# Optimization experiments

Hardware: AMD Instinct MI355X
Metric: run time of the kernel (lower is better)

Reference implementation:

```python
import jax, jax.numpy as jnp
import numpy as np

T, C, H, W, D = 100, 2, 128, 128, 8192


def setup_inputs() -> dict:
    key = jax.random.key(0)
    k1, k2, k3, k4 = jax.random.split(key, 4)
    # event histogram: nonnegative intensities per (time, polarity, y, x)
    hist = jax.random.uniform(k1, (T, C, H, W), dtype=jnp.float32)
    # torchhd Random(vsa='MAP') tables are random bipolar {-1,+1} vectors
    time_w = jnp.sign(jax.random.normal(k2, (T, D), dtype=jnp.float32))
    pol_w = jnp.sign(jax.random.normal(k3, (C, D), dtype=jnp.float32))
    pos_w = jnp.sign(jax.random.normal(k4, (H * W, D), dtype=jnp.float32))
    return {"hist": hist, "time_w": time_w, "pol_w": pol_w, "pos_w": pos_w}


def reference(hist, time_w, pol_w, pos_w):
    # Original: for every nonzero pixel, bind (elementwise mul in MAP)
    # pos_hv * pol_hv * time_hv, scale by intensity, accumulate, then sign.
    # Equivalent fused form:
    #   out_d = sign( sum_{t,p,n} hist[t,p,n] * pos_w[n,d] * pol_w[p,d] * time_w[t,d] )
    t, c, h, w = hist.shape
    flat = hist.reshape(t, c, h * w)                      # [T, 2, H*W]
    # intensity-weighted sum of position HVs per (t, p): one GEMM over H*W
    acc = jnp.einsum('tpn,nd->tpd', flat, pos_w)          # [T, 2, D]
    # bind with polarity and time HVs, reduce over t and p
    gesture = jnp.einsum('tpd,pd,td->d', acc, pol_w, time_w)  # [D]
    return jnp.sign(gesture)
```

## Files before the change

### kernel.cpp

```cpp
#include <hip/hip_runtime.h>
#include <cstdint>
#include <cstddef>

#define TT    100
#define MROWS 200
#define KDIM  16384
#define DDIM  8192
#define KSL   16
#define KPER  (KDIM / KSL)

typedef __bf16 bf16x8 __attribute__((ext_vector_type(8)));
typedef float  f32x4  __attribute__((ext_vector_type(4)));

static __device__ __forceinline__ unsigned short f2bf_rne(float f) {
    unsigned int u = __float_as_uint(f);
    unsigned int r = (u + 0x7FFFu + ((u >> 16) & 1u)) >> 16;
    return (unsigned short)r;
}
static __device__ __forceinline__ float bf2f(unsigned short s) {
    return __uint_as_float(((unsigned int)s) << 16);
}

__global__ __launch_bounds__(256) void zero_kernel(float* __restrict__ out) {
    out[blockIdx.x * 256 + threadIdx.x] = 0.f;
}

__global__ __launch_bounds__(256) void gemm_kernel(const float* __restrict__ hist,
                                                   const float* __restrict__ pos,
                                                   const float* __restrict__ time_w,
                                                   const float* __restrict__ pol_w,
                                                   float* __restrict__ out) {
    __shared__ alignas(16) unsigned short As[2][128][32];
    __shared__ alignas(16) unsigned short Bs[128][40];
    __shared__ float sPart[128];

    const int t     = threadIdx.x;
    const int n0    = blockIdx.x * 128;
    const int m0    = blockIdx.y * 128;
    const int kbase = blockIdx.z * KPER;

    const int lane = t & 63;
    const int wv   = t >> 6;
    const int wm   = (wv & 1) * 64;
    const int wn   = (wv >> 1) * 64;
    const int l15  = lane & 15;
    const int q8   = (lane >> 4) * 8;

    if (t < 128) sPart[t] = 0.f;

    const int ar  = t >> 2;
    const int akb = (t & 3) * 8;
    const int rowA0 = m0 + ar;
    const int rowA1 = m0 + ar + 64;
    const bool v0 = rowA0 < MROWS;
    const bool v1 = rowA1 < MROWS;
    const float* gA0 = hist + (size_t)rowA0 * KDIM + akb;
    const float* gA1 = hist + (size_t)rowA1 * KDIM + akb;

    const int bk2 = (t & 15) * 2;
    const int bnb = (t >> 4) * 8;
    const float* gB0 = pos + ((size_t)kbase + bk2) * DDIM + n0 + bnb;
    const float* gB1 = gB0 + DDIM;

    f32x4 acc[4][4];
#pragma unroll
    for (int s = 0; s < 4; ++s)
#pragma unroll
        for (int j = 0; j < 4; ++j) acc[s][j] = (f32x4){0.f, 0.f, 0.f, 0.f};

    for (int kk = 0; kk < KPER; kk += 32) {
        float4 a00 = {0,0,0,0}, a01 = {0,0,0,0};
        float4 a10 = {0,0,0,0}, a11 = {0,0,0,0};
        if (v0) { a00 = *(const float4*)(gA0 + kbase + kk);
                  a01 = *(const float4*)(gA0 + kbase + kk + 4); }
        if (v1) { a10 = *(const float4*)(gA1 + kbase + kk);
                  a11 = *(const float4*)(gA1 + kbase + kk + 4); }
        const float* b0 = gB0 + (size_t)kk * DDIM;
        const float* b1 = gB1 + (size_t)kk * DDIM;
        float4 x0 = *(const float4*)(b0);
        float4 x1 = *(const float4*)(b0 + 4);
        float4 y0 = *(const float4*)(b1);
        float4 y1 = *(const float4*)(b1 + 4);

        __syncthreads();

        {
            float va[8] = {a00.x, a00.y, a00.z, a00.w, a01.x, a01.y, a01.z, a01.w};
            float vb[8] = {a10.x, a10.y, a10.z, a10.w, a11.x, a11.y, a11.z, a11.w};
            alignas(16) unsigned short h0[8], l0[8], h1[8], l1[8];
#pragma unroll
            for (int i = 0; i < 8; ++i) {
                unsigned short h = f2bf_rne(va[i]);
                h0[i] = h; l0[i] = f2bf_rne(va[i] - bf2f(h));
                unsigned short g = f2bf_rne(vb[i]);
                h1[i] = g; l1[i] = f2bf_rne(vb[i] - bf2f(g));
            }
            *(uint4*)&As[0][ar][akb]      = *(const uint4*)h0;
            *(uint4*)&As[1][ar][akb]      = *(const uint4*)l0;
            *(uint4*)&As[0][ar + 64][akb] = *(const uint4*)h1;
            *(uint4*)&As[1][ar + 64][akb] = *(const uint4*)l1;
        }
        {
            const float xv[8] = {x0.x, x0.y, x0.z, x0.w, x1.x, x1.y, x1.z, x1.w};
            const float yv[8] = {y0.x, y0.y, y0.z, y0.w, y1.x, y1.y, y1.z, y1.w};
#pragma unroll
            for (int j = 0; j < 8; ++j) {
                unsigned int w = (__float_as_uint(xv[j]) >> 16) |
                                 (__float_as_uint(yv[j]) & 0xFFFF0000u);
                *(unsigned int*)&Bs[bnb + j][bk2] = w;
            }
        }

        __syncthreads();

        uint4 fa0[4], fa1[4], fb[4];
#pragma unroll
        for (int s = 0; s < 4; ++s) {
            fa0[s] = *(const uint4*)&As[0][wm + s * 16 + l15][q8];
            fa1[s] = *(const uint4*)&As[1][wm + s * 16 + l15][q8];
        }
#pragma unroll
        for (int j = 0; j < 4; ++j)
            fb[j] = *(const uint4*)&Bs[wn + j * 16 + l15][q8];

#pragma unroll
        for (int s = 0; s < 4; ++s)
#pragma unroll
            for (int j = 0; j < 4; ++j) {
                acc[s][j] = __builtin_amdgcn_mfma_f32_16x16x32_bf16(
                    __builtin_bit_cast(bf16x8, fa0[s]),
                    __builtin_bit_cast(bf16x8, fb[j]), acc[s][j], 0, 0, 0);
                acc[s][j] = __builtin_amdgcn_mfma_f32_16x16x32_bf16(
                    __builtin_bit_cast(bf16x8, fa1[s]),
                    __builtin_bit_cast(bf16x8, fb[j]), acc[s][j], 0, 0, 0);
            }
    }

    const int qrow = (lane >> 4) * 4;
#pragma unroll
    for (int j = 0; j < 4; ++j) {
        const int col = wn + j * 16 + l15;
        const int d   = n0 + col;
        const float p0 = pol_w[d];
        const float p1 = pol_w[DDIM + d];
        float part = 0.f;
#pragma unroll
        for (int s = 0; s < 4; ++s)
#pragma unroll
            for (int r = 0; r < 4; ++r) {
                const int m = m0 + wm + s * 16 + qrow + r;
                if (m < MROWS) {
                    const int tt_ = m >> 1;
                    const float w = time_w[(size_t)tt_ * DDIM + d] *
                                    ((m & 1) ? p1 : p0);
                    part += w * acc[s][j][r];
                }
            }
        atomicAdd(&sPart[col], part);
    }
    __syncthreads();
    if (t < 128) atomicAdd(out + n0 + t, sPart[t]);
}

__global__ __launch_bounds__(256) void sign_kernel(float* __restrict__ out) {
    int d = blockIdx.x * 256 + threadIdx.x;
    float s = out[d];
    out[d] = (s > 0.f) ? 1.f : ((s < 0.f) ? -1.f : 0.f);
}

extern "C" void kernel_launch(void* const* d_in, const int* in_sizes, int n_in,
                              void* d_out, int out_size, void* d_ws, size_t ws_size,
                              hipStream_t stream) {
    const float* hist   = (const float*)d_in[0];
    const float* time_w = (const float*)d_in[1];
    const float* pol_w  = (const float*)d_in[2];
    const float* pos_w  = (const float*)d_in[3];
    float* out = (float*)d_out;
    (void)d_ws; (void)ws_size;

    zero_kernel<<<DDIM / 256, 256, 0, stream>>>(out);
    gemm_kernel<<<dim3(DDIM / 128, 2, KSL), 256, 0, stream>>>(hist, pos_w, time_w, pol_w, out);
    sign_kernel<<<DDIM / 256, 256, 0, stream>>>(out);
}
```

Baseline: 767.7 us.

## Precompute bf16 hi/lo split of hist and cover all M rows per block

A new prep kernel converts hist once into swizzled bf16 hi/lo planes padded to 224 rows in workspace. The GEMM then tiles all rows in a single block (M=224), so pos_w is streamed once instead of twice, and the A tiles are loaded directly into LDS with global_load_lds, using an XOR swizzle to avoid bank conflicts. The grid is reordered so k-slices vary fastest. The cost is an extra kernel launch plus a workspace round trip, and a larger accumulator (7x4 tiles) that raises register pressure.

```diff
diff --git a/kernel.cpp b/kernel.cpp
--- a/kernel.cpp
+++ b/kernel.cpp
@@ -2,12 +2,13 @@
 #include <cstdint>
 #include <cstddef>
 
-#define TT    100
 #define MROWS 200
+#define PM    224
 #define KDIM  16384
 #define DDIM  8192
 #define KSL   16
 #define KPER  (KDIM / KSL)
+#define BK    32
 
 typedef __bf16 bf16x8 __attribute__((ext_vector_type(8)));
 typedef float  f32x4  __attribute__((ext_vector_type(4)));
@@ -21,60 +22,96 @@
     return __uint_as_float(((unsigned int)s) << 16);
 }
 
+static __device__ __forceinline__ void gld_lds16(const unsigned short* g,
+                                                 unsigned short* l) {
+    __builtin_amdgcn_global_load_lds(
+        (const __attribute__((address_space(1))) unsigned int*)g,
+        (__attribute__((address_space(3))) unsigned int*)l, 16, 0, 0);
+}
+
 __global__ __launch_bounds__(256) void zero_kernel(float* __restrict__ out) {
     out[blockIdx.x * 256 + threadIdx.x] = 0.f;
 }
 
-__global__ __launch_bounds__(256) void gemm_kernel(const float* __restrict__ hist,
-                                                   const float* __restrict__ pos,
-                                                   const float* __restrict__ time_w,
-                                                   const float* __restrict__ pol_w,
-                                                   float* __restrict__ out) {
-    __shared__ alignas(16) unsigned short As[2][128][32];
+__global__ __launch_bounds__(256) void prep_kernel(const float* __restrict__ hist,
+                                                   unsigned short* __restrict__ ahi,
+                                                   unsigned short* __restrict__ alo) {
+    const int g  = blockIdx.x * 256 + threadIdx.x;
+    const int m  = g >> 11;
+    const int gc = g & 2047;
+    const int f  = (m >> 1) & 3;
+    const int sgc = (gc & ~3) | ((gc & 3) ^ f);
+    alignas(16) unsigned short hi[8], lo[8];
+    if (m < MROWS) {
+        const float* src = hist + (size_t)m * KDIM + sgc * 8;
+        float4 a = *(const float4*)(src);
+        float4 b = *(const float4*)(src + 4);
+        const float v[8] = {a.x, a.y, a.z, a.w, b.x, b.y, b.z, b.w};
+#pragma unroll
+        for (int i = 0; i < 8; ++i) {
+            unsigned short h = f2bf_rne(v[i]);
+            hi[i] = h;
+            lo[i] = f2bf_rne(v[i] - bf2f(h));
+        }
+    } else {
+#pragma unroll
+        for (int i = 0; i < 8; ++i) { hi[i] = 0; lo[i] = 0; }
+    }
+    *(uint4*)(ahi + (size_t)g * 8) = *(const uint4*)hi;
+    *(uint4*)(alo + (size_t)g * 8) = *(const uint4*)lo;
+}
+
+__global__ __launch_bounds__(256, 2)
+void gemm_kernel(const unsigned short* __restrict__ ahi,
+                 const unsigned short* __restrict__ alo,
+                 const float* __restrict__ pos,
+                 const float* __restrict__ time_w,
+                 const float* __restrict__ pol_w,
+                 float* __restrict__ out) {
+    __shared__ alignas(16) unsigned short As0[PM * BK];
+    __shared__ alignas(16) unsigned short As1[PM * BK];
     __shared__ alignas(16) unsigned short Bs[128][40];
     __shared__ float sPart[128];
 
     const int t     = threadIdx.x;
-    const int n0    = blockIdx.x * 128;
-    const int m0    = blockIdx.y * 128;
-    const int kbase = blockIdx.z * KPER;
+    const int ks    = blockIdx.x;
+    const int n0    = blockIdx.y * 128;
+    const int kbase = ks * KPER;
 
     const int lane = t & 63;
     const int wv   = t >> 6;
-    const int wm   = (wv & 1) * 64;
+    const int wm   = (wv & 1) * 112;
     const int wn   = (wv >> 1) * 64;
     const int l15  = lane & 15;
     const int q8   = (lane >> 4) * 8;
+    const int qg   = (lane >> 4) ^ ((l15 >> 1) & 3);
 
     if (t < 128) sPart[t] = 0.f;
 
-    const int ar  = t >> 2;
-    const int akb = (t & 3) * 8;
-    const int rowA0 = m0 + ar;
-    const int rowA1 = m0 + ar + 64;
-    const bool v0 = rowA0 < MROWS;
-    const bool v1 = rowA1 < MROWS;
-    const float* gA0 = hist + (size_t)rowA0 * KDIM + akb;
-    const float* gA1 = hist + (size_t)rowA1 * KDIM + akb;
+    const int lr = lane >> 2, lg = lane & 3;
+    const unsigned short* gA[7];
+    unsigned short* lA[7];
+#pragma unroll
+    for (int i = 0; i < 7; ++i) {
+        const int cc = wv * 7 + i;
+        const int pl = (cc >= 14) ? 1 : 0;
+        const int ch = cc - pl * 14;
+        gA[i] = (pl ? alo : ahi) + (size_t)(ch * 16 + lr) * KDIM + kbase + lg * 8;
+        lA[i] = (pl ? As1 : As0) + ch * 512;
+    }
 
     const int bk2 = (t & 15) * 2;
     const int bnb = (t >> 4) * 8;
     const float* gB0 = pos + ((size_t)kbase + bk2) * DDIM + n0 + bnb;
     const float* gB1 = gB0 + DDIM;
 
-    f32x4 acc[4][4];
-#pragma unroll
-    for (int s = 0; s < 4; ++s)
+    f32x4 acc[7][4];
+#pragma unroll
+    for (int s = 0; s < 7; ++s)
 #pragma unroll
         for (int j = 0; j < 4; ++j) acc[s][j] = (f32x4){0.f, 0.f, 0.f, 0.f};
 
-    for (int kk = 0; kk < KPER; kk += 32) {
-        float4 a00 = {0,0,0,0}, a01 = {0,0,0,0};
-        float4 a10 = {0,0,0,0}, a11 = {0,0,0,0};
-        if (v0) { a00 = *(const float4*)(gA0 + kbase + kk);
-                  a01 = *(const float4*)(gA0 + kbase + kk + 4); }
-        if (v1) { a10 = *(const float4*)(gA1 + kbase + kk);
-                  a11 = *(const float4*)(gA1 + kbase + kk + 4); }
+    for (int kk = 0; kk < KPER; kk += BK) {
         const float* b0 = gB0 + (size_t)kk * DDIM;
         const float* b1 = gB1 + (size_t)kk * DDIM;
         float4 x0 = *(const float4*)(b0);
@@ -84,22 +121,9 @@
 
         __syncthreads();
 
-        {
-            float va[8] = {a00.x, a00.y, a00.z, a00.w, a01.x, a01.y, a01.z, a01.w};
-            float vb[8] = {a10.x, a10.y, a10.z, a10.w, a11.x, a11.y, a11.z, a11.w};
-            alignas(16) unsigned short h0[8], l0[8], h1[8], l1[8];
-#pragma unroll
-            for (int i = 0; i < 8; ++i) {
-                unsigned short h = f2bf_rne(va[i]);
-                h0[i] = h; l0[i] = f2bf_rne(va[i] - bf2f(h));
-                unsigned short g = f2bf_rne(vb[i]);
-                h1[i] = g; l1[i] = f2bf_rne(vb[i] - bf2f(g));
-            }
-            *(uint4*)&As[0][ar][akb]      = *(const uint4*)h0;
-            *(uint4*)&As[1][ar][akb]      = *(const uint4*)l0;
-            *(uint4*)&As[0][ar + 64][akb] = *(const uint4*)h1;
-            *(uint4*)&As[1][ar + 64][akb] = *(const uint4*)l1;
-        }
+#pragma unroll
+        for (int i = 0; i < 7; ++i) gld_lds16(gA[i] + kk, lA[i]);
+
         {
             const float xv[8] = {x0.x, x0.y, x0.z, x0.w, x1.x, x1.y, x1.z, x1.w};
             const float yv[8] = {y0.x, y0.y, y0.z, y0.w, y1.x, y1.y, y1.z, y1.w};
@@ -113,27 +137,26 @@
 
         __syncthreads();
 
-        uint4 fa0[4], fa1[4], fb[4];
-#pragma unroll
-        for (int s = 0; s < 4; ++s) {
-            fa0[s] = *(const uint4*)&As[0][wm + s * 16 + l15][q8];
-            fa1[s] = *(const uint4*)&As[1][wm + s * 16 + l15][q8];
-        }
+        uint4 fb[4];
 #pragma unroll
         for (int j = 0; j < 4; ++j)
             fb[j] = *(const uint4*)&Bs[wn + j * 16 + l15][q8];
 
 #pragma unroll
-        for (int s = 0; s < 4; ++s)
+        for (int s = 0; s < 7; ++s) {
+            const int mr = wm + s * 16 + l15;
+            const uint4 fa0 = *(const uint4*)&As0[mr * 32 + qg * 8];
+            const uint4 fa1 = *(const uint4*)&As1[mr * 32 + qg * 8];
 #pragma unroll
             for (int j = 0; j < 4; ++j) {
                 acc[s][j] = __builtin_amdgcn_mfma_f32_16x16x32_bf16(
-                    __builtin_bit_cast(bf16x8, fa0[s]),
+                    __builtin_bit_cast(bf16x8, fa0),
                     __builtin_bit_cast(bf16x8, fb[j]), acc[s][j], 0, 0, 0);
                 acc[s][j] = __builtin_amdgcn_mfma_f32_16x16x32_bf16(
-                    __builtin_bit_cast(bf16x8, fa1[s]),
+                    __builtin_bit_cast(bf16x8, fa1),
                     __builtin_bit_cast(bf16x8, fb[j]), acc[s][j], 0, 0, 0);
             }
+        }
     }
 
     const int qrow = (lane >> 4) * 4;
@@ -145,13 +168,12 @@
         const float p1 = pol_w[DDIM + d];
         float part = 0.f;
 #pragma unroll
-        for (int s = 0; s < 4; ++s)
+        for (int s = 0; s < 7; ++s)
 #pragma unroll
             for (int r = 0; r < 4; ++r) {
-                const int m = m0 + wm + s * 16 + qrow + r;
+                const int m = wm + s * 16 + qrow + r;
                 if (m < MROWS) {
-                    const int tt_ = m >> 1;
-                    const float w = time_w[(size_t)tt_ * DDIM + d] *
+                    const float w = time_w[(size_t)(m >> 1) * DDIM + d] *
                                     ((m & 1) ? p1 : p0);
                     part += w * acc[s][j][r];
                 }
@@ -176,9 +198,14 @@
     const float* pol_w  = (const float*)d_in[2];
     const float* pos_w  = (const float*)d_in[3];
     float* out = (float*)d_out;
-    (void)d_ws; (void)ws_size;
+
+    unsigned short* ahi = (unsigned short*)d_ws;
+    unsigned short* alo = ahi + (size_t)PM * KDIM;
+    (void)in_sizes; (void)n_in; (void)out_size; (void)ws_size;
 
     zero_kernel<<<DDIM / 256, 256, 0, stream>>>(out);
-    gemm_kernel<<<dim3(DDIM / 128, 2, KSL), 256, 0, stream>>>(hist, pos_w, time_w, pol_w, out);
+    prep_kernel<<<(PM * (KDIM / 8)) / 256, 256, 0, stream>>>(hist, ahi, alo);
+    gemm_kernel<<<dim3(KSL, DDIM / 128), 256, 0, stream>>>(ahi, alo, pos_w,
+                                                           time_w, pol_w, out);
     sign_kernel<<<DDIM / 256, 256, 0, stream>>>(out);
 }
```

Result: faster. 752.1 us (-2.0%).
